# Optimization experiments

Measured on AMD Instinct MI355X. Metric: run time of the kernel, lower is better.

Reference implementation:

```python
import jax, jax.numpy as jnp
import numpy as np

B = 1024      # batch
G = 2000      # num_genes
S = 32        # uniform per-gene feature width (geneid_num[i] == 32 for all i)
M1, M2, M3 = 4096, 2048, 1024  # mul_len1/2/3
H = 64        # hidden width of all small MLPs


def setup_inputs() -> dict:
    key = jax.random.key(0)
    ks = jax.random.split(key, 24)
    n = lambda k, shape, s=0.02: jax.random.normal(k, shape, dtype=jnp.float32) * s
    return {
        # activations
        "x":  jax.random.normal(ks[0], (B, G * S), dtype=jnp.float32),
        "z1": jax.random.normal(ks[1], (B, M1), dtype=jnp.float32),
        "z2": jax.random.normal(ks[2], (B, M2), dtype=jnp.float32),
        "z3": jax.random.normal(ks[3], (B, M3), dtype=jnp.float32),
        # per-gene Linear(S,1) weights, stacked: block-diagonal gene stage
        "Wg": n(ks[4], (G, S)), "bg": n(ks[5], (G,)),
        # fc0: Linear(G, 64); fc1/2/3: Linear(Mi, 64). Layout (in, out).
        "W0": n(ks[6], (G, H)),  "b0": n(ks[7], (H,)),
        "W1": n(ks[8], (M1, H)), "b1": n(ks[9], (H,)),
        "W2": n(ks[10], (M2, H)), "b2": n(ks[11], (H,)),
        "W3": n(ks[12], (M3, H)), "b3": n(ks[13], (H,)),
        # learned fusion weights (init 0.5 in torch)
        "w1": jnp.full((H,), 0.5, jnp.float32),
        "w2": jnp.full((H,), 0.5, jnp.float32),
        "w3": jnp.full((H,), 0.5, jnp.float32),
        # final fc: 64->64->64->1
        "fW1": n(ks[14], (H, H)), "fb1": n(ks[15], (H,)),
        "fW2": n(ks[16], (H, H)), "fb2": n(ks[17], (H,)),
        "fW3": n(ks[18], (H, 1)), "fb3": n(ks[19], (1,)),
    }


def reference(x, z1, z2, z3, Wg, bg, W0, b0, W1, b1, W2, b2, W3, b3,
              w1, w2, w3, fW1, fb1, fW2, fb2, fW3, fb3):
    g, s = Wg.shape
    b = x.shape[0]
    # ragged per-gene Linear(numi,1)+ReLU loop == block-diagonal contraction
    # x: [B, G*S] -> [B, G, S]; gene_outputs: [B, G]
    gene = jax.nn.relu(jnp.einsum('bgs,gs->bg', x.reshape(b, g, s), Wg) + bg)
    h0 = jax.nn.relu(gene @ W0 + b0)                 # fc0(gene_outputs)  [B, 64]
    d1 = jax.nn.relu(z1 @ W1 + b1) * w1 + h0         # fc1(z1)*weights_1 + fc0
    d2 = jax.nn.relu(z2 @ W2 + b2) * w2 + d1         # fc2(z2)*weights_2 + d1
    d3 = jax.nn.relu(z3 @ W3 + b3) * w3 + d2         # fc3(z3)*weights_3 + d2
    h = jax.nn.relu(d3 @ fW1 + fb1)
    h = jax.nn.relu(h @ fW2 + fb2)
    return h @ fW3 + fb3                             # [B, 1]
```

## Files before the change

### kernel.cpp

```cpp
#include <hip/hip_runtime.h>

constexpr int BB = 1024;
constexpr int GG = 2000;
constexpr int SS = 32;
constexpr int K1 = 4096, K2 = 2048, K3 = 1024;

constexpr int BH = BB * 64;

constexpr int Y1P_OFF = 0;
constexpr int Y2P_OFF = 4 * BH;
constexpr int Y3P_OFF = 6 * BH;
constexpr int HP_OFF  = 7 * BH;

constexpr int NCH       = 63;
constexpr int NGENE_BLK = NCH * 16;
constexpr int NGEMM_BLK = 224;
constexpr int KCH       = 1024;

__global__ __launch_bounds__(256, 4) void k1_gene_fc0_zgemm(
    const float* __restrict__ x,  const float* __restrict__ z1,
    const float* __restrict__ z2, const float* __restrict__ z3,
    const float* __restrict__ Wg, const float* __restrict__ bg,
    const float* __restrict__ W0,
    const float* __restrict__ W1, const float* __restrict__ W2,
    const float* __restrict__ W3, float* __restrict__ ws)
{
    __shared__ float lds[64 * 32];
    const int bid = blockIdx.x;
    const int t   = threadIdx.x;
    const int per = bid / 11;
    const int off = bid % 11;

    if (off >= 2) {
        const int gid   = per * 9 + (off - 2);
        const int chunk = gid % NCH;
        const int bgrp  = gid / NCH;
        const int g0    = chunk * 32;
        const int b0    = bgrp * 64;
        const int g     = g0 + (t >> 3);
        const bool gv   = (g < GG);

        float4 wg4 = make_float4(0.f, 0.f, 0.f, 0.f);
        if (gv) wg4 = ((const float4*)Wg)[g0 * 8 + t];
        const float bias = (gv && (t & 7) == 0) ? bg[g] : 0.f;

        const float* xp = gv ? (x + (size_t)b0 * (GG * SS) + g0 * SS + t * 4)
                             : x;
        float* gS = lds;

        #pragma unroll 4
        for (int i = 0; i < 64; ++i) {
            float4 x4 = *(const float4*)(xp + (size_t)i * (GG * SS));
            float p = x4.x * wg4.x + x4.y * wg4.y + x4.z * wg4.z + x4.w * wg4.w;
            p += __shfl_xor(p, 1);
            p += __shfl_xor(p, 2);
            p += __shfl_xor(p, 4);
            if ((t & 7) == 0)
                gS[i * 32 + (t >> 3)] = gv ? fmaxf(p + bias, 0.f) : 0.f;
        }

        const int n = t & 63;
        const int w = t >> 6;
        float w0r[32];
        #pragma unroll
        for (int j = 0; j < 32; ++j) {
            int gj = g0 + j; if (gj >= GG) gj = GG - 1;
            w0r[j] = W0[(size_t)gj * 64 + n];
        }
        __syncthreads();

        float* hp = ws + HP_OFF + (size_t)chunk * BH + (size_t)b0 * 64;
        #pragma unroll 4
        for (int mi = 0; mi < 16; ++mi) {
            const int m = w * 16 + mi;
            float acc = 0.f;
            #pragma unroll
            for (int jj = 0; jj < 8; ++jj) {
                const float4 g4 = *(const float4*)&gS[m * 32 + jj * 4];
                acc = fmaf(g4.w, w0r[jj * 4 + 3], fmaf(g4.z, w0r[jj * 4 + 2],
                      fmaf(g4.y, w0r[jj * 4 + 1], fmaf(g4.x, w0r[jj * 4 + 0], acc))));
            }
            hp[(size_t)m * 64 + n] = acc;
        }
    } else {
        const int id = per * 2 + off;
        const float* z; const float* W; int K; int mt; int kslab; float* ys;
        if (id < 128)      { z = z1; W = W1; K = K1; mt = id >> 2; kslab = id & 3;
                             ys = ws + Y1P_OFF + (size_t)kslab * BH; }
        else if (id < 192) { int l = id - 128; z = z2; W = W2; K = K2; mt = l >> 1; kslab = l & 1;
                             ys = ws + Y2P_OFF + (size_t)kslab * BH; }
        else               { int l = id - 192; z = z3; W = W3; K = K3; mt = l; kslab = 0;
                             ys = ws + Y3P_OFF; }

        const int m0    = mt * 32;
        const int kbase = kslab * KCH;
        const int n2    = t & 31;
        const int mq    = t >> 5;
        float* zt = lds;

        float2 acc[4];
        #pragma unroll
        for (int j = 0; j < 4; ++j) acc[j] = make_float2(0.f, 0.f);

        for (int kc = 0; kc < KCH / 64; ++kc) {
            const int k0 = kbase + kc * 64;
            {
                const int i0 = t, i1 = t + 256;
                ((float4*)zt)[i0] = *(const float4*)&z[(size_t)(m0 + (i0 >> 4)) * K + k0 + (i0 & 15) * 4];
                ((float4*)zt)[i1] = *(const float4*)&z[(size_t)(m0 + (i1 >> 4)) * K + k0 + (i1 & 15) * 4];
            }
            __syncthreads();
            #pragma unroll
            for (int kk = 0; kk < 64; kk += 4) {
                const float* Wp = &W[(size_t)(k0 + kk) * 64 + n2 * 2];
                const float2 wv0 = *(const float2*)(Wp);
                const float2 wv1 = *(const float2*)(Wp + 64);
                const float2 wv2 = *(const float2*)(Wp + 128);
                const float2 wv3 = *(const float2*)(Wp + 192);
                #pragma unroll
                for (int j = 0; j < 4; ++j) {
                    const float4 zj = *(const float4*)&zt[(mq * 4 + j) * 64 + kk];
                    acc[j].x = fmaf(zj.x, wv0.x, acc[j].x); acc[j].y = fmaf(zj.x, wv0.y, acc[j].y);
                    acc[j].x = fmaf(zj.y, wv1.x, acc[j].x); acc[j].y = fmaf(zj.y, wv1.y, acc[j].y);
                    acc[j].x = fmaf(zj.z, wv2.x, acc[j].x); acc[j].y = fmaf(zj.z, wv2.y, acc[j].y);
                    acc[j].x = fmaf(zj.w, wv3.x, acc[j].x); acc[j].y = fmaf(zj.w, wv3.y, acc[j].y);
                }
            }
            __syncthreads();
        }
        #pragma unroll
        for (int j = 0; j < 4; ++j)
            *(float2*)&ys[(size_t)(m0 + mq * 4 + j) * 64 + n2 * 2] = acc[j];
    }
}

__global__ __launch_bounds__(256, 4) void k2_combine_mlp(
    const float* __restrict__ ws,
    const float* __restrict__ b0v,
    const float* __restrict__ b1v, const float* __restrict__ b2v,
    const float* __restrict__ b3v,
    const float* __restrict__ w1v, const float* __restrict__ w2v,
    const float* __restrict__ w3v,
    const float* __restrict__ fW1, const float* __restrict__ fb1,
    const float* __restrict__ fW2, const float* __restrict__ fb2,
    const float* __restrict__ fW3, const float* __restrict__ fb3,
    float* __restrict__ out)
{
    const float* Y1p = ws + Y1P_OFF;
    const float* Y2p = ws + Y2P_OFF;
    const float* Y3p = ws + Y3P_OFF;

    const int t   = threadIdx.x;
    const int n   = t & 63;
    const int w   = t >> 6;
    const int row = blockIdx.x * 4 + w;
    const int rn  = row * 64 + n;

    float h = 0.f;
    const float* hp = ws + HP_OFF + rn;
    #pragma unroll 9
    for (int c = 0; c < NCH; ++c) h += hp[(size_t)c * BH];
    const float h0 = fmaxf(h + b0v[n], 0.f);

    const float y1 = Y1p[rn] + Y1p[BH + rn] + Y1p[2 * BH + rn] + Y1p[3 * BH + rn];
    float d = fmaf(fmaxf(y1 + b1v[n], 0.f), w1v[n], h0);
    const float y2 = Y2p[rn] + Y2p[BH + rn];
    d = fmaf(fmaxf(y2 + b2v[n], 0.f), w2v[n], d);
    const float y3 = Y3p[rn];
    d = fmaf(fmaxf(y3 + b3v[n], 0.f), w3v[n], d);

    __shared__ float sd[4][64];
    __shared__ float sh[4][64];
    sd[w][n] = d;
    __syncthreads();
    float a1 = fb1[n];
    #pragma unroll 8
    for (int j = 0; j < 64; ++j) a1 = fmaf(sd[w][j], fW1[j * 64 + n], a1);
    a1 = fmaxf(a1, 0.f);
    sh[w][n] = a1;
    __syncthreads();
    float a2 = fb2[n];
    #pragma unroll 8
    for (int j = 0; j < 64; ++j) a2 = fmaf(sh[w][j], fW2[j * 64 + n], a2);
    a2 = fmaxf(a2, 0.f);

    float v = a2 * fW3[n];
    #pragma unroll
    for (int o = 32; o > 0; o >>= 1) v += __shfl_xor(v, o);
    if (n == 0) out[row] = v + fb3[0];
}

extern "C" void kernel_launch(void* const* d_in, const int* in_sizes, int n_in,
                              void* d_out, int out_size, void* d_ws, size_t ws_size,
                              hipStream_t stream)
{
    const float* x   = (const float*)d_in[0];
    const float* z1  = (const float*)d_in[1];
    const float* z2  = (const float*)d_in[2];
    const float* z3  = (const float*)d_in[3];
    const float* Wg  = (const float*)d_in[4];
    const float* bg  = (const float*)d_in[5];
    const float* W0  = (const float*)d_in[6];
    const float* b0v = (const float*)d_in[7];
    const float* W1  = (const float*)d_in[8];
    const float* b1v = (const float*)d_in[9];
    const float* W2  = (const float*)d_in[10];
    const float* b2v = (const float*)d_in[11];
    const float* W3  = (const float*)d_in[12];
    const float* b3v = (const float*)d_in[13];
    const float* w1v = (const float*)d_in[14];
    const float* w2v = (const float*)d_in[15];
    const float* w3v = (const float*)d_in[16];
    const float* fW1 = (const float*)d_in[17];
    const float* fb1 = (const float*)d_in[18];
    const float* fW2 = (const float*)d_in[19];
    const float* fb2 = (const float*)d_in[20];
    const float* fW3 = (const float*)d_in[21];
    const float* fb3 = (const float*)d_in[22];

    float* ws  = (float*)d_ws;
    float* out = (float*)d_out;

    k1_gene_fc0_zgemm<<<dim3(NGENE_BLK + NGEMM_BLK), dim3(256), 0, stream>>>(
        x, z1, z2, z3, Wg, bg, W0, W1, W2, W3, ws);

    k2_combine_mlp<<<dim3(BB / 4), dim3(256), 0, stream>>>(
        ws, b0v, b1v, b2v, b3v, w1v, w2v, w3v,
        fW1, fb1, fW2, fb2, fW3, fb3, out);
}
```

Before: 488.0 us.

## Split gene blocks finer, batch x loads, stage W tiles in LDS

Halves the batch rows each gene block handles (32 instead of 64), doubling the gene block count, and raises the launch-bounds occupancy hint to 8 blocks. The x-row loads are issued eight at a time into registers before the shuffle reductions, to raise memory-level parallelism on the dominant x stream. The z-GEMM blocks now stage each 64x64 W tile into LDS instead of reading W from global inside the inner loop. The interleaved block mapping is replaced by running GEMM blocks first, then gene blocks. The cost is that W0 is reloaded by twice as many gene blocks, LDS use per block grows, and register pressure rises under the tighter occupancy hint.

New measurement: 426.0 us. 1.15x faster.

```diff
diff --git a/kernel.cpp b/kernel.cpp
--- a/kernel.cpp
+++ b/kernel.cpp
@@ -13,11 +13,11 @@
 constexpr int HP_OFF  = 7 * BH;
 
 constexpr int NCH       = 63;
-constexpr int NGENE_BLK = NCH * 16;
+constexpr int NGENE_BLK = NCH * 32;
 constexpr int NGEMM_BLK = 224;
 constexpr int KCH       = 1024;
 
-__global__ __launch_bounds__(256, 4) void k1_gene_fc0_zgemm(
+__global__ __launch_bounds__(256, 8) void k1_gene_fc0_zgemm(
     const float* __restrict__ x,  const float* __restrict__ z1,
     const float* __restrict__ z2, const float* __restrict__ z3,
     const float* __restrict__ Wg, const float* __restrict__ bg,
@@ -25,18 +25,16 @@
     const float* __restrict__ W1, const float* __restrict__ W2,
     const float* __restrict__ W3, float* __restrict__ ws)
 {
-    __shared__ float lds[64 * 32];
+    __shared__ float lds[6144];
     const int bid = blockIdx.x;
     const int t   = threadIdx.x;
-    const int per = bid / 11;
-    const int off = bid % 11;
-
-    if (off >= 2) {
-        const int gid   = per * 9 + (off - 2);
+
+    if (bid >= NGEMM_BLK) {
+        const int gid   = bid - NGEMM_BLK;
         const int chunk = gid % NCH;
         const int bgrp  = gid / NCH;
         const int g0    = chunk * 32;
-        const int b0    = bgrp * 64;
+        const int b0    = bgrp * 32;
         const int g     = g0 + (t >> 3);
         const bool gv   = (g < GG);
 
@@ -48,15 +46,21 @@
                              : x;
         float* gS = lds;
 
-        #pragma unroll 4
-        for (int i = 0; i < 64; ++i) {
-            float4 x4 = *(const float4*)(xp + (size_t)i * (GG * SS));
-            float p = x4.x * wg4.x + x4.y * wg4.y + x4.z * wg4.z + x4.w * wg4.w;
-            p += __shfl_xor(p, 1);
-            p += __shfl_xor(p, 2);
-            p += __shfl_xor(p, 4);
-            if ((t & 7) == 0)
-                gS[i * 32 + (t >> 3)] = gv ? fmaxf(p + bias, 0.f) : 0.f;
+        for (int ii = 0; ii < 32; ii += 8) {
+            float4 xr[8];
+            #pragma unroll
+            for (int j = 0; j < 8; ++j)
+                xr[j] = *(const float4*)(xp + (size_t)(ii + j) * (GG * SS));
+            #pragma unroll
+            for (int j = 0; j < 8; ++j) {
+                float p = (xr[j].x * wg4.x + xr[j].y * wg4.y)
+                        + (xr[j].z * wg4.z + xr[j].w * wg4.w);
+                p += __shfl_xor(p, 1);
+                p += __shfl_xor(p, 2);
+                p += __shfl_xor(p, 4);
+                if ((t & 7) == 0)
+                    gS[(ii + j) * 32 + (t >> 3)] = gv ? fmaxf(p + bias, 0.f) : 0.f;
+            }
         }
 
         const int n = t & 63;
@@ -70,9 +74,9 @@
         __syncthreads();
 
         float* hp = ws + HP_OFF + (size_t)chunk * BH + (size_t)b0 * 64;
-        #pragma unroll 4
-        for (int mi = 0; mi < 16; ++mi) {
-            const int m = w * 16 + mi;
+        #pragma unroll
+        for (int mi = 0; mi < 8; ++mi) {
+            const int m = w * 8 + mi;
             float acc = 0.f;
             #pragma unroll
             for (int jj = 0; jj < 8; ++jj) {
@@ -83,7 +87,7 @@
             hp[(size_t)m * 64 + n] = acc;
         }
     } else {
-        const int id = per * 2 + off;
+        const int id = bid;
         const float* z; const float* W; int K; int mt; int kslab; float* ys;
         if (id < 128)      { z = z1; W = W1; K = K1; mt = id >> 2; kslab = id & 3;
                              ys = ws + Y1P_OFF + (size_t)kslab * BH; }
@@ -97,6 +101,7 @@
         const int n2    = t & 31;
         const int mq    = t >> 5;
         float* zt = lds;
+        float* wt = lds + 2048;
 
         float2 acc[4];
         #pragma unroll
@@ -108,15 +113,22 @@
                 const int i0 = t, i1 = t + 256;
                 ((float4*)zt)[i0] = *(const float4*)&z[(size_t)(m0 + (i0 >> 4)) * K + k0 + (i0 & 15) * 4];
                 ((float4*)zt)[i1] = *(const float4*)&z[(size_t)(m0 + (i1 >> 4)) * K + k0 + (i1 & 15) * 4];
+                #pragma unroll
+                for (int r = 0; r < 4; ++r) {
+                    const int idx = t + r * 256;
+                    const int row = idx >> 4;
+                    const int c4  = (idx & 15) * 4;
+                    *(float4*)&wt[row * 64 + c4] =
+                        *(const float4*)&W[(size_t)(k0 + row) * 64 + c4];
+                }
             }
             __syncthreads();
             #pragma unroll
             for (int kk = 0; kk < 64; kk += 4) {
-                const float* Wp = &W[(size_t)(k0 + kk) * 64 + n2 * 2];
-                const float2 wv0 = *(const float2*)(Wp);
-                const float2 wv1 = *(const float2*)(Wp + 64);
-                const float2 wv2 = *(const float2*)(Wp + 128);
-                const float2 wv3 = *(const float2*)(Wp + 192);
+                const float2 wv0 = *(const float2*)&wt[(kk + 0) * 64 + n2 * 2];
+                const float2 wv1 = *(const float2*)&wt[(kk + 1) * 64 + n2 * 2];
+                const float2 wv2 = *(const float2*)&wt[(kk + 2) * 64 + n2 * 2];
+                const float2 wv3 = *(const float2*)&wt[(kk + 3) * 64 + n2 * 2];
                 #pragma unroll
                 for (int j = 0; j < 4; ++j) {
                     const float4 zj = *(const float4*)&zt[(mq * 4 + j) * 64 + kk];
@@ -221,7 +233,7 @@
     float* ws  = (float*)d_ws;
     float* out = (float*)d_out;
 
-    k1_gene_fc0_zgemm<<<dim3(NGENE_BLK + NGEMM_BLK), dim3(256), 0, stream>>>(
+    k1_gene_fc0_zgemm<<<dim3(NGEMM_BLK + NGENE_BLK), dim3(256), 0, stream>>>(
         x, z1, z2, z3, Wg, bg, W0, W1, W2, W3, ws);
 
     k2_combine_mlp<<<dim3(BB / 4), dim3(256), 0, stream>>>(
```
